# Optimization experiments

Measured on AMD Instinct MI355X. Metric: run time of the kernel, lower is better.

Reference implementation:

```python
import jax, jax.numpy as jnp
import numpy as np

FFT_LEN = 512
HOP = 256
WIN_LEN = 1024


def setup_inputs() -> dict:
    key = jax.random.key(0)
    k1, k2 = jax.random.split(key)
    inputs = jax.random.normal(k1, (8, 514, 4000), dtype=jnp.float32)
    win = jax.random.uniform(k2, (WIN_LEN,), dtype=jnp.float32)
    return {"inputs": inputs, "win": win}


def reference(inputs, win):
    B, D, T = inputs.shape  # D == 514
    half = FFT_LEN // 2  # 256
    real = inputs[:, :half, :]            # [B,256,T]
    imag = inputs[:, half + 1:-1, :]      # [B,256,T]
    c = jax.lax.complex(real, imag)       # bins 0..255
    # conjugate-symmetric extension: bin 256 = 0, bins 257..511 = conj(bins 255..1)
    tail = jnp.conj(jnp.flip(c[:, 1:, :], axis=1))            # [B,255,T]
    zero = jnp.zeros_like(c[:, :1, :])
    spec = jnp.concatenate([c, zero, tail], axis=1)           # [B,512,T]
    # torch does fft over the freq axis and keeps the real part
    ifft_data = jnp.real(jnp.fft.fft(spec, axis=1)).astype(jnp.float32)  # [B,512,T]
    tmp = jnp.concatenate([ifft_data, ifft_data], axis=1)     # [B,1024,T]
    tmp = tmp * win[None, :, None] * 256.0
    # overlap-add via four shifted padded copies (faithful to the original)
    t1 = jnp.pad(tmp, ((0, 0), (0, 768), (0, 3)))
    t2 = jnp.pad(tmp, ((0, 0), (256, 512), (1, 2)))
    t3 = jnp.pad(tmp, ((0, 0), (512, 256), (2, 1)))
    t4 = jnp.pad(tmp, ((0, 0), (768, 0), (3, 0)))
    synbuf = t1 + t2 + t3 + t4                                # [B,1792,T+3]
    syn = synbuf[:, 768:1024, :-4]                            # [B,256,T-1]
    syn = jnp.flip(syn, axis=1)
    syn = jnp.transpose(syn, (0, 2, 1)).reshape(B, -1)        # [B,256*(T-1)]
    return syn
```

## Files before the change

### kernel.cpp

```cpp
#include <hip/hip_runtime.h>


typedef __attribute__((ext_vector_type(8))) short short8;
typedef __attribute__((ext_vector_type(8))) __bf16 bf16x8;
typedef __attribute__((ext_vector_type(4))) float floatx4;

__device__ inline short f2bf(float f) {
  unsigned u = __builtin_bit_cast(unsigned, f);
  u = (u + 0x7fffu + ((u >> 16) & 1u)) >> 16;
  return (short)(unsigned short)u;
}

#define PI_OVER_256 0.01227184630308513f

__global__ void build_m(short* __restrict__ M) {
  int idx = blockIdx.x * blockDim.x + threadIdx.x;
  int ntile = idx >> 10;
  int s = (idx >> 6) & 15;
  int lane = idx & 63;
  int n = ntile * 16 + (lane & 15);
  int kb = lane >> 4;
  short8 v;
#pragma unroll
  for (int e = 0; e < 8; e++) {
    int kap = s * 32 + kb * 8 + e;
    int gk = 2 * (kap & 255) + (kap >> 8);
    float val;
    if (gk == 0) {
      val = 1.0f;
    } else if (gk < 256) {
      int m = (n * gk) & 511;
      val = 2.0f * __cosf((float)m * PI_OVER_256);
    } else {
      int m = (n * (gk - 256)) & 511;
      val = 2.0f * __sinf((float)m * PI_OVER_256);
    }
    v[e] = f2bf(val);
  }
  ((short8*)M)[idx] = v;
}

__global__ __launch_bounds__(512) void gemm_ola(
    const float* __restrict__ in, const float* __restrict__ win,
    const short* __restrict__ M, float* __restrict__ out) {
  __shared__ short ldsX[32 * 512];

  const int tid = threadIdx.x;
  const int b = blockIdx.y;
  const int tile = blockIdx.x;
  const int c0 = 28 * tile - 4;

  {
    const int cbase = 4 * (tid & 7);
    const int kap0 = (tid >> 3) * 8;
    const int gc = c0 + cbase;
    floatx4 f[8];
    if (gc >= 0 && gc <= 3996) {
      const float* src = in + (size_t)b * 2056000 + gc;
#pragma unroll
      for (int j = 0; j < 8; j++) {
        int kap = kap0 + j;
        int gk = 2 * (kap & 255) + (kap >> 8);
        int row = (gk < 256) ? gk : gk + 1;
        f[j] = *(const floatx4*)(src + (size_t)row * 4000);
      }
    } else {
#pragma unroll
      for (int j = 0; j < 8; j++) f[j] = floatx4{0.f, 0.f, 0.f, 0.f};
    }
    const int g = kap0 >> 3;
#pragma unroll
    for (int cc = 0; cc < 4; cc++) {
      short8 v;
#pragma unroll
      for (int j = 0; j < 8; j++) v[j] = f2bf(f[j][cc]);
      const int col = cbase + cc;
      *(short8*)&ldsX[col * 512 + ((g ^ (col & 7)) << 3)] = v;
    }
  }
  __syncthreads();

  const int w = tid >> 6;
  const int lane = tid & 63;
  const int c = lane & 15;
  const int kb = lane >> 4;
  const int rg = kb;

  floatx4 accE[2][2] = {};
  floatx4 accO[2][2] = {};

  const short8* Mf = (const short8*)M;
  const int J0 = 2 * w, J1 = 2 * w + 1;

  bf16x8 cb0 = __builtin_bit_cast(bf16x8, Mf[(J0 * 16 + 0) * 64 + lane]);
  bf16x8 cb1 = __builtin_bit_cast(bf16x8, Mf[(J1 * 16 + 0) * 64 + lane]);

#pragma unroll
  for (int s = 0; s < 16; s++) {
    bf16x8 nb0, nb1;
    if (s < 15) {
      nb0 = __builtin_bit_cast(bf16x8, Mf[(J0 * 16 + s + 1) * 64 + lane]);
      nb1 = __builtin_bit_cast(bf16x8, Mf[(J1 * 16 + s + 1) * 64 + lane]);
    }
    const int g = 4 * s + kb;
    const int col0 = c;
    const int col1 = 16 + c;
    bf16x8 a0 = __builtin_bit_cast(
        bf16x8, *(const short8*)&ldsX[col0 * 512 + ((g ^ (col0 & 7)) << 3)]);
    bf16x8 a1 = __builtin_bit_cast(
        bf16x8, *(const short8*)&ldsX[col1 * 512 + ((g ^ (col1 & 7)) << 3)]);
    if (s < 8) {
      accE[0][0] = __builtin_amdgcn_mfma_f32_16x16x32_bf16(a0, cb0, accE[0][0], 0, 0, 0);
      accE[0][1] = __builtin_amdgcn_mfma_f32_16x16x32_bf16(a0, cb1, accE[0][1], 0, 0, 0);
      accE[1][0] = __builtin_amdgcn_mfma_f32_16x16x32_bf16(a1, cb0, accE[1][0], 0, 0, 0);
      accE[1][1] = __builtin_amdgcn_mfma_f32_16x16x32_bf16(a1, cb1, accE[1][1], 0, 0, 0);
    } else {
      accO[0][0] = __builtin_amdgcn_mfma_f32_16x16x32_bf16(a0, cb0, accO[0][0], 0, 0, 0);
      accO[0][1] = __builtin_amdgcn_mfma_f32_16x16x32_bf16(a0, cb1, accO[0][1], 0, 0, 0);
      accO[1][0] = __builtin_amdgcn_mfma_f32_16x16x32_bf16(a1, cb0, accO[1][0], 0, 0, 0);
      accO[1][1] = __builtin_amdgcn_mfma_f32_16x16x32_bf16(a1, cb1, accO[1][1], 0, 0, 0);
    }
    if (s < 15) { cb0 = nb0; cb1 = nb1; }
  }

#pragma unroll
  for (int jt = 0; jt < 2; jt++) {
    const int J = 2 * w + jt;
    const int j = 16 * J + c;
    const float wv0 = 256.0f * win[768 + j];
    const float wv1 = 256.0f * win[512 + j];
    const float wv2 = 256.0f * win[256 + j];
    const float wv3 = 256.0f * win[j];

    floatx4 Y[2], Yh[2];
#pragma unroll
    for (int q = 0; q < 2; q++) {
      Y[q] = accE[q][jt] + accO[q][jt];
      Yh[q] = accE[q][jt] - accO[q][jt];
    }

#pragma unroll
    for (int q = 0; q < 2; q++) {
      const int qm = (q > 0) ? q - 1 : 0;
      float yb[4], yhb[4];
#pragma unroll
      for (int p = 1; p < 4; p++) {
        float ia = __shfl(Y[q][p], lane - 16, 64);
        float pa = __shfl(Y[qm][p], lane + 48, 64);
        yb[p] = (rg > 0) ? ia : pa;
      }
#pragma unroll
      for (int p = 2; p < 4; p++) {
        float ia = __shfl(Yh[q][p], lane - 16, 64);
        float pa = __shfl(Yh[qm][p], lane + 48, 64);
        yhb[p] = (rg > 0) ? ia : pa;
      }
      floatx4 v;
#pragma unroll
      for (int p = 0; p < 4; p++) {
        float t1 = (p >= 1) ? Y[q][p - 1] : yb[3];
        float t2 = (p >= 2) ? Yh[q][p - 2] : yhb[p + 2];
        float t3 = (p >= 3) ? Y[q][p - 3] : yb[p + 1];
        v[p] = wv0 * Yh[q][p] + wv1 * t1 + wv2 * t2 + wv3 * t3;
      }
#pragma unroll
      for (int p = 0; p < 4; p++) {
        const int L = 16 * q + 4 * rg + p;
        const int t = c0 + L;
        if (L >= 4 && t <= 3998) {
          out[((size_t)b * 3999 + t) * 256 + (255 - j)] = v[p];
        }
      }
    }
  }
}

extern "C" void kernel_launch(void* const* d_in, const int* in_sizes, int n_in,
                              void* d_out, int out_size, void* d_ws, size_t ws_size,
                              hipStream_t stream) {
  const float* in = (const float*)d_in[0];
  const float* win = (const float*)d_in[1];
  float* out = (float*)d_out;
  short* M = (short*)d_ws;

  hipLaunchKernelGGL(build_m, dim3(64), dim3(256), 0, stream, M);
  hipLaunchKernelGGL(gemm_ola, dim3(143, 8), dim3(512), 0, stream, in, win, M, out);
}
```

Baseline: 120.9 us.

## Deepen operand prefetch, rework LDS swizzle, halve shuffles, remap grid batch-fastest

The MFMA loop now prefetches cosine-matrix fragments two steps ahead and LDS activation fragments one step ahead, so load latency overlaps the matrix ops. The LDS swizzle changes from XOR to an additive rotation, and bf16 packing is written as paired 32-bit words. The overlap-add boundary exchange selects its source before shuffling, which halves the cross-lane shuffles. The grid is flattened so consecutive blocks cover different batches of the same time tile, and the launch bounds now request 4 blocks per CU. In exchange, more registers are held live for prefetch, which could run into the occupancy hint.

```diff
diff --git a/kernel.cpp b/kernel.cpp
--- a/kernel.cpp
+++ b/kernel.cpp
@@ -4,11 +4,17 @@
 typedef __attribute__((ext_vector_type(8))) short short8;
 typedef __attribute__((ext_vector_type(8))) __bf16 bf16x8;
 typedef __attribute__((ext_vector_type(4))) float floatx4;
-
-__device__ inline short f2bf(float f) {
+typedef __attribute__((ext_vector_type(4))) unsigned uintx4;
+
+__device__ inline unsigned bfbits(float f) {
   unsigned u = __builtin_bit_cast(unsigned, f);
-  u = (u + 0x7fffu + ((u >> 16) & 1u)) >> 16;
-  return (short)(unsigned short)u;
+  return (u + 0x7fffu + ((u >> 16) & 1u)) >> 16;
+}
+
+__device__ inline short f2bf(float f) { return (short)(unsigned short)bfbits(f); }
+
+__device__ inline unsigned pk2bf(float a, float b) {
+  return (bfbits(a) & 0xffffu) | (bfbits(b) << 16);
 }
 
 #define PI_OVER_256 0.01227184630308513f
@@ -40,19 +46,25 @@
   ((short8*)M)[idx] = v;
 }
 
-__global__ __launch_bounds__(512) void gemm_ola(
+__device__ inline int lds_off(int col, int g) {
+  return col * 512 + (((g & 56) | ((g + col) & 7)) << 3);
+}
+
+__global__ __launch_bounds__(512, 4) void gemm_ola(
     const float* __restrict__ in, const float* __restrict__ win,
     const short* __restrict__ M, float* __restrict__ out) {
   __shared__ short ldsX[32 * 512];
 
   const int tid = threadIdx.x;
-  const int b = blockIdx.y;
-  const int tile = blockIdx.x;
+  const int bid = blockIdx.x;
+  const int b = bid & 7;
+  const int tile = bid >> 3;
   const int c0 = 28 * tile - 4;
 
   {
     const int cbase = 4 * (tid & 7);
-    const int kap0 = (tid >> 3) * 8;
+    const int gg = tid >> 3;
+    const int kap0 = gg * 8;
     const int gc = c0 + cbase;
     floatx4 f[8];
     if (gc >= 0 && gc <= 3996) {
@@ -68,14 +80,13 @@
 #pragma unroll
       for (int j = 0; j < 8; j++) f[j] = floatx4{0.f, 0.f, 0.f, 0.f};
     }
-    const int g = kap0 >> 3;
 #pragma unroll
     for (int cc = 0; cc < 4; cc++) {
-      short8 v;
-#pragma unroll
-      for (int j = 0; j < 8; j++) v[j] = f2bf(f[j][cc]);
       const int col = cbase + cc;
-      *(short8*)&ldsX[col * 512 + ((g ^ (col & 7)) << 3)] = v;
+      uintx4 u;
+#pragma unroll
+      for (int i = 0; i < 4; i++) u[i] = pk2bf(f[2 * i][cc], f[2 * i + 1][cc]);
+      *(uintx4*)&ldsX[lds_off(col, gg)] = u;
     }
   }
   __syncthreads();
@@ -92,35 +103,38 @@
   const short8* Mf = (const short8*)M;
   const int J0 = 2 * w, J1 = 2 * w + 1;
 
-  bf16x8 cb0 = __builtin_bit_cast(bf16x8, Mf[(J0 * 16 + 0) * 64 + lane]);
-  bf16x8 cb1 = __builtin_bit_cast(bf16x8, Mf[(J1 * 16 + 0) * 64 + lane]);
+  bf16x8 c00 = __builtin_bit_cast(bf16x8, Mf[(J0 * 16 + 0) * 64 + lane]);
+  bf16x8 c01 = __builtin_bit_cast(bf16x8, Mf[(J1 * 16 + 0) * 64 + lane]);
+  bf16x8 n00 = __builtin_bit_cast(bf16x8, Mf[(J0 * 16 + 1) * 64 + lane]);
+  bf16x8 n01 = __builtin_bit_cast(bf16x8, Mf[(J1 * 16 + 1) * 64 + lane]);
+  bf16x8 a0 = __builtin_bit_cast(bf16x8, *(const short8*)&ldsX[lds_off(c, kb)]);
+  bf16x8 a1 = __builtin_bit_cast(bf16x8, *(const short8*)&ldsX[lds_off(16 + c, kb)]);
 
 #pragma unroll
   for (int s = 0; s < 16; s++) {
-    bf16x8 nb0, nb1;
+    bf16x8 f00, f01, na0, na1;
+    if (s < 14) {
+      f00 = __builtin_bit_cast(bf16x8, Mf[(J0 * 16 + s + 2) * 64 + lane]);
+      f01 = __builtin_bit_cast(bf16x8, Mf[(J1 * 16 + s + 2) * 64 + lane]);
+    }
     if (s < 15) {
-      nb0 = __builtin_bit_cast(bf16x8, Mf[(J0 * 16 + s + 1) * 64 + lane]);
-      nb1 = __builtin_bit_cast(bf16x8, Mf[(J1 * 16 + s + 1) * 64 + lane]);
-    }
-    const int g = 4 * s + kb;
-    const int col0 = c;
-    const int col1 = 16 + c;
-    bf16x8 a0 = __builtin_bit_cast(
-        bf16x8, *(const short8*)&ldsX[col0 * 512 + ((g ^ (col0 & 7)) << 3)]);
-    bf16x8 a1 = __builtin_bit_cast(
-        bf16x8, *(const short8*)&ldsX[col1 * 512 + ((g ^ (col1 & 7)) << 3)]);
+      const int g = 4 * (s + 1) + kb;
+      na0 = __builtin_bit_cast(bf16x8, *(const short8*)&ldsX[lds_off(c, g)]);
+      na1 = __builtin_bit_cast(bf16x8, *(const short8*)&ldsX[lds_off(16 + c, g)]);
+    }
     if (s < 8) {
-      accE[0][0] = __builtin_amdgcn_mfma_f32_16x16x32_bf16(a0, cb0, accE[0][0], 0, 0, 0);
-      accE[0][1] = __builtin_amdgcn_mfma_f32_16x16x32_bf16(a0, cb1, accE[0][1], 0, 0, 0);
-      accE[1][0] = __builtin_amdgcn_mfma_f32_16x16x32_bf16(a1, cb0, accE[1][0], 0, 0, 0);
-      accE[1][1] = __builtin_amdgcn_mfma_f32_16x16x32_bf16(a1, cb1, accE[1][1], 0, 0, 0);
+      accE[0][0] = __builtin_amdgcn_mfma_f32_16x16x32_bf16(a0, c00, accE[0][0], 0, 0, 0);
+      accE[0][1] = __builtin_amdgcn_mfma_f32_16x16x32_bf16(a0, c01, accE[0][1], 0, 0, 0);
+      accE[1][0] = __builtin_amdgcn_mfma_f32_16x16x32_bf16(a1, c00, accE[1][0], 0, 0, 0);
+      accE[1][1] = __builtin_amdgcn_mfma_f32_16x16x32_bf16(a1, c01, accE[1][1], 0, 0, 0);
     } else {
-      accO[0][0] = __builtin_amdgcn_mfma_f32_16x16x32_bf16(a0, cb0, accO[0][0], 0, 0, 0);
-      accO[0][1] = __builtin_amdgcn_mfma_f32_16x16x32_bf16(a0, cb1, accO[0][1], 0, 0, 0);
-      accO[1][0] = __builtin_amdgcn_mfma_f32_16x16x32_bf16(a1, cb0, accO[1][0], 0, 0, 0);
-      accO[1][1] = __builtin_amdgcn_mfma_f32_16x16x32_bf16(a1, cb1, accO[1][1], 0, 0, 0);
-    }
-    if (s < 15) { cb0 = nb0; cb1 = nb1; }
+      accO[0][0] = __builtin_amdgcn_mfma_f32_16x16x32_bf16(a0, c00, accO[0][0], 0, 0, 0);
+      accO[0][1] = __builtin_amdgcn_mfma_f32_16x16x32_bf16(a0, c01, accO[0][1], 0, 0, 0);
+      accO[1][0] = __builtin_amdgcn_mfma_f32_16x16x32_bf16(a1, c00, accO[1][0], 0, 0, 0);
+      accO[1][1] = __builtin_amdgcn_mfma_f32_16x16x32_bf16(a1, c01, accO[1][1], 0, 0, 0);
+    }
+    c00 = n00; c01 = n01; n00 = f00; n01 = f01;
+    a0 = na0; a1 = na1;
   }
 
 #pragma unroll
@@ -145,15 +159,13 @@
       float yb[4], yhb[4];
 #pragma unroll
       for (int p = 1; p < 4; p++) {
-        float ia = __shfl(Y[q][p], lane - 16, 64);
-        float pa = __shfl(Y[qm][p], lane + 48, 64);
-        yb[p] = (rg > 0) ? ia : pa;
+        float z = (rg == 3) ? Y[qm][p] : Y[q][p];
+        yb[p] = __shfl(z, lane + 48, 64);
       }
 #pragma unroll
       for (int p = 2; p < 4; p++) {
-        float ia = __shfl(Yh[q][p], lane - 16, 64);
-        float pa = __shfl(Yh[qm][p], lane + 48, 64);
-        yhb[p] = (rg > 0) ? ia : pa;
+        float z = (rg == 3) ? Yh[qm][p] : Yh[q][p];
+        yhb[p] = __shfl(z, lane + 48, 64);
       }
       floatx4 v;
 #pragma unroll
@@ -184,5 +196,5 @@
   short* M = (short*)d_ws;
 
   hipLaunchKernelGGL(build_m, dim3(64), dim3(256), 0, stream, M);
-  hipLaunchKernelGGL(gemm_ola, dim3(143, 8), dim3(512), 0, stream, in, win, M, out);
-}
+  hipLaunchKernelGGL(gemm_ola, dim3(1144), dim3(512), 0, stream, in, win, M, out);
+}
```

Result: no change. 121.0 us (+0.1%).
